# Kernel optimization log

Hardware: AMD Instinct MI355X
Metric: run time of the kernel (lower is better)

The kernel has to match this reference:

```python
import jax, jax.numpy as jnp
import numpy as np

V, D, B, T = 50257, 512, 64, 512
MEM, FWD = 64, 48
RETRO = MEM - FWD  # 16
EPS = 1e-5


def setup_inputs() -> dict:
    key = jax.random.key(0)
    ks = jax.random.split(key, 16)
    n = lambda i, shape: (jax.random.normal(ks[i], shape, jnp.float32) * 0.02)
    return dict(
        seq=jax.random.randint(ks[0], (B, T), 0, V),
        embed=n(1, (V, D)),
        ff_w1=n(2, (D, 2 * D)), ff_b1=jnp.zeros((2 * D,), jnp.float32),
        ff_w2=n(3, (2 * D, D)), ff_b2=jnp.zeros((D,), jnp.float32),
        ln_g=jnp.ones((D,), jnp.float32), ln_b=jnp.zeros((D,), jnp.float32),
        fg_w=n(4, (D,)), fg_b=jnp.zeros((), jnp.float32),
        nw_w1=n(5, (2 * D, D)), nw_b1=jnp.zeros((D,), jnp.float32),
        nw_w2=n(6, (D,)), nw_b2=jnp.zeros((), jnp.float32),
        wq=n(7, (D, D)), bq=jnp.zeros((D,), jnp.float32),
        wk=n(8, (D, D)), bk=jnp.zeros((D,), jnp.float32),
        wv=n(9, (D, D)), bv=jnp.zeros((D,), jnp.float32),
        wo=n(10, (D, D)), bo=jnp.zeros((D,), jnp.float32),
        rq_w=n(11, (D, D)), rq_b=jnp.zeros((D,), jnp.float32),
        out_w=n(12, (D, V)), out_b=jnp.zeros((V,), jnp.float32),
    )


def reference(seq, embed, ff_w1, ff_b1, ff_w2, ff_b2, ln_g, ln_b,
              fg_w, fg_b, nw_w1, nw_b1, nw_w2, nw_b2,
              wq, bq, wk, bk, wv, bv, wo, bo, rq_w, rq_b, out_w, out_b):
    Bz = seq.shape[0]
    # Encoder: embed -> FFN residual -> LayerNorm
    h0 = embed[seq]                                            # [B,T,D]
    ff = jax.nn.relu(h0 @ ff_w1 + ff_b1) @ ff_w2 + ff_b2
    x = h0 + ff
    mu = x.mean(-1, keepdims=True)
    var = ((x - mu) ** 2).mean(-1, keepdims=True)
    hidden = (x - mu) / jnp.sqrt(var + EPS) * ln_g + ln_b       # [B,T,D]

    cand = hidden[:, :-3, :]                                   # [B,n_cand,D]
    n_cand = cand.shape[1]
    # Forward-gate topk (sorted ascending, as in torch code)
    fwd_scores = cand @ fg_w + fg_b                            # [B,n_cand]
    _, fwd_idx = jax.lax.top_k(fwd_scores, FWD)
    fwd_idx = jnp.sort(fwd_idx, axis=1)                        # [B,FWD]
    fwd_h = jnp.take_along_axis(hidden, fwd_idx[:, :, None], axis=1)  # [B,FWD,D]

    # Condition 'D': MHA re-encode (1 head) of forward slots over full sequence
    q = fwd_h @ wq + bq                                        # [B,FWD,D]
    kk = hidden @ wk + bk                                      # [B,T,D]
    v = hidden @ wv + bv                                       # [B,T,D]
    attn = jax.nn.softmax(jnp.einsum('bkd,btd->bkt', q, kk) / jnp.sqrt(jnp.float32(D)), axis=-1)
    re_slots = jnp.einsum('bkt,btd->bkd', attn, v) @ wo + bo   # [B,FWD,D]

    # New-write gate over skipped candidates -> retro slots
    context = hidden.mean(1)                                   # [B,D]
    gi = jnp.concatenate([cand, jnp.broadcast_to(context[:, None, :], cand.shape)], axis=-1)
    gs = jax.nn.sigmoid(jax.nn.relu(gi @ nw_w1 + nw_b1) @ nw_w2 + nw_b2)  # [B,n_cand]
    fwd_mask = jnp.zeros((Bz, n_cand), jnp.float32).at[
        jnp.arange(Bz)[:, None], fwd_idx].set(1.0)
    masked = jnp.where(fwd_mask > 0, -1e9, gs)
    _, sel = jax.lax.top_k(masked, RETRO)                      # [B,RETRO], descending-score order
    retro_h = jnp.take_along_axis(hidden, sel[:, :, None], axis=1)  # [B,RETRO,D]

    memory = jnp.concatenate([re_slots, retro_h], axis=1)      # [B,MEM,D] (exactly full)
    mem_mask = jnp.ones((Bz, MEM), jnp.float32)

    # Read head
    qh = hidden[:, -2, :] @ rq_w + rq_b                        # [B,D]
    scores = jnp.einsum('bmd,bd->bm', memory, qh)
    scores = jnp.where(mem_mask == 0, -1e9, scores)
    a = jax.nn.softmax(scores, axis=-1)
    ctx = jnp.einsum('bm,bmd->bd', a, memory)
    return ctx @ out_w + out_b                                 # [B,V]
```

## Files before the change

kernel.cpp:

```cpp
#include <hip/hip_runtime.h>

typedef unsigned short u16;
typedef unsigned int u32;

#define VV 50257
#define NCAND 509
#define NFWD 48
#define NRETRO 16

typedef __attribute__((ext_vector_type(8))) short bf16x8;
typedef __attribute__((ext_vector_type(4))) float f32x4;

__device__ __forceinline__ float bf2f(u16 u) {
  union { u32 i; float f; } v; v.i = ((u32)u) << 16; return v.f;
}
__device__ __forceinline__ u16 f2bf(float f) {
  union { float f; u32 u; } v; v.f = f;
  u32 u = v.u; u += 0x7fffu + ((u >> 16) & 1u); return (u16)(u >> 16);
}
__device__ __forceinline__ u16 bft(float f) {
  union { float f; u32 u; } v; v.f = f; return (u16)(v.u >> 16);
}
__device__ __forceinline__ float ldsel(const void* p, size_t i, int isbf) {
  return isbf ? bf2f(((const u16*)p)[i]) : ((const float*)p)[i];
}

__device__ __forceinline__ void g2l16(const u16* g, u16* l) {
  __builtin_amdgcn_global_load_lds((const __attribute__((address_space(1))) u32*)g,
                                   (__attribute__((address_space(3))) u32*)l, 16, 0, 0);
}

__global__ void detect_k(const u32* __restrict__ w, int* __restrict__ flag) {
  int bf = 1;
  for (int i = 0; i < 16; ++i) {
    u32 b1 = (w[i] >> 8) & 0x7fu;
    if (!(b1 >= 0x30u && b1 < 0x40u)) bf = 0;
  }
  *flag = bf;
}

__global__ void sentinel_k(float* __restrict__ out, int n, float val) {
  int i = blockIdx.x * 256 + threadIdx.x;
  if (i < n) out[i] = val;
}

__global__ __launch_bounds__(256) void tsplit_k(const float* __restrict__ W,
                                                u16* __restrict__ Th, u16* __restrict__ Tl,
                                                int K, int N) {
  __shared__ float tt[32][33];
  int nt = N >> 5;
  int n0 = (blockIdx.x % nt) << 5;
  int k0 = (blockIdx.x / nt) << 5;
  int c = threadIdx.x & 31, r = threadIdx.x >> 5;
#pragma unroll
  for (int i = 0; i < 32; i += 8) tt[r + i][c] = W[(size_t)(k0 + r + i) * N + n0 + c];
  __syncthreads();
#pragma unroll
  for (int i = 0; i < 32; i += 8) {
    int n = n0 + r + i, k = k0 + c;
    float v = tt[c][r + i];
    u16 h = bft(v);
    int idx = n * K + (k & ~63) + ((k & 63) ^ ((n & 7) << 3));
    Th[idx] = h; Tl[idx] = f2bf(v - bf2f(h));
  }
}

__global__ __launch_bounds__(256) void gsplit_k(const float* __restrict__ embed,
                                                const int* __restrict__ seqp,
                                                u16* __restrict__ Ph, u16* __restrict__ Pl) {
  int g = blockIdx.x * 256 + threadIdx.x;
  int m = g >> 6, j8 = (g & 63) << 3;
  const float* s = embed + (size_t)seqp[m] * 512 + j8;
  float4 a = *(const float4*)s;
  float4 b = *(const float4*)(s + 4);
  u16 h0 = bft(a.x), h1 = bft(a.y), h2 = bft(a.z), h3 = bft(a.w);
  u16 h4 = bft(b.x), h5 = bft(b.y), h6 = bft(b.z), h7 = bft(b.w);
  uint4 hv, lv;
  hv.x = (u32)h0 | ((u32)h1 << 16); hv.y = (u32)h2 | ((u32)h3 << 16);
  hv.z = (u32)h4 | ((u32)h5 << 16); hv.w = (u32)h6 | ((u32)h7 << 16);
  lv.x = (u32)f2bf(a.x - bf2f(h0)) | ((u32)f2bf(a.y - bf2f(h1)) << 16);
  lv.y = (u32)f2bf(a.z - bf2f(h2)) | ((u32)f2bf(a.w - bf2f(h3)) << 16);
  lv.z = (u32)f2bf(b.x - bf2f(h4)) | ((u32)f2bf(b.y - bf2f(h5)) << 16);
  lv.w = (u32)f2bf(b.z - bf2f(h6)) | ((u32)f2bf(b.w - bf2f(h7)) << 16);
  int di = m * 512 + (j8 ^ ((m & 7) << 3));
  *(uint4*)&Ph[di] = hv;
  *(uint4*)&Pl[di] = lv;
}

template<int ADDM, int RELU, int ACC, int OUT>
__global__ __launch_bounds__(256) void mgemm_k(
    const u16* __restrict__ Ah, const u16* __restrict__ Al,
    const u16* __restrict__ Bh, const u16* __restrict__ Bl,
    int ldk, int koff,
    const float* __restrict__ biasf, int boff,
    const u16* __restrict__ Rh, const u16* __restrict__ Rl,
    const float* __restrict__ addf,
    float* __restrict__ Cf, u16* __restrict__ Cb,
    u16* __restrict__ Ohi, u16* __restrict__ Olo)
{
  __shared__ __align__(16) u16 lds[32768];
  int tid = threadIdx.x;
  int cpx = gridDim.x >> 3;
  int bid = blockIdx.x;
  int wg = (bid & 7) * cpx + (bid >> 3);
  int my = wg >> 2, nx = wg & 3;
  int m0 = my << 7, n0 = nx << 7;
  int lane = tid & 63, wid = tid >> 6;

  const u16* gw; int stw;
  if (wid == 0)      { gw = Ah + (size_t)m0 * 512;        stw = 512; }
  else if (wid == 1) { gw = Al + (size_t)m0 * 512;        stw = 512; }
  else if (wid == 2) { gw = Bh + (size_t)n0 * ldk + koff; stw = ldk; }
  else               { gw = Bl + (size_t)n0 * ldk + koff; stw = ldk; }
  const u16* gl = gw + (size_t)(lane >> 3) * stw + ((lane & 7) << 3);
  int lb = wid << 13;

  f32x4 acc[4][4] = {};
  int wr = wid >> 1, wc = wid & 1;
  int cl = lane & 15;
  int kq8 = (lane >> 4) << 3;
  int swz = (cl & 7) << 3;

  for (int k0 = 0; k0 < 512; k0 += 64) {
#pragma unroll
    for (int i = 0; i < 16; ++i)
      g2l16(gl + (size_t)(i << 3) * stw + k0, &lds[lb + (i << 9)]);
    __syncthreads();
#pragma unroll
    for (int kt = 0; kt < 2; ++kt) {
      int kA = ((kt << 5) + kq8) ^ swz;
      bf16x8 bh[4], blo[4];
#pragma unroll
      for (int i = 0; i < 4; ++i) {
        int ib = (((wc << 6) + (i << 4) + cl) << 6) + kA;
        bh[i]  = *(const bf16x8*)&lds[16384 + ib];
        blo[i] = *(const bf16x8*)&lds[24576 + ib];
      }
#pragma unroll
      for (int i2 = 0; i2 < 4; ++i2) {
        int ia = (((wr << 6) + (i2 << 4) + cl) << 6) + kA;
        bf16x8 ah  = *(const bf16x8*)&lds[ia];
        bf16x8 alo = *(const bf16x8*)&lds[8192 + ia];
#pragma unroll
        for (int j = 0; j < 4; ++j) {
          acc[i2][j] = __builtin_amdgcn_mfma_f32_16x16x32_bf16(ah,  bh[j],  acc[i2][j], 0, 0, 0);
          acc[i2][j] = __builtin_amdgcn_mfma_f32_16x16x32_bf16(alo, bh[j],  acc[i2][j], 0, 0, 0);
          acc[i2][j] = __builtin_amdgcn_mfma_f32_16x16x32_bf16(ah,  blo[j], acc[i2][j], 0, 0, 0);
        }
      }
    }
    __syncthreads();
  }

  int rq = (lane >> 4) << 2;
  int mb = m0 + (wr << 6);
  int nb = n0 + (wc << 6);
#pragma unroll
  for (int j = 0; j < 4; ++j) {
    int n = nb + (j << 4) + cl;
    float bi = biasf ? biasf[boff + n] : 0.f;
#pragma unroll
    for (int i2 = 0; i2 < 4; ++i2) {
#pragma unroll
      for (int r = 0; r < 4; ++r) {
        int m = mb + (i2 << 4) + rq + r;
        float v = acc[i2][j][r] + bi;
        if (ADDM == 1) {
          int ridx = m * 512 + (n ^ ((m & 7) << 3));
          v += bf2f(Rh[ridx]) + bf2f(Rl[ridx]);
        }
        if (ADDM == 2) v += addf[((m >> 9) << 9) + n];
        if (ACC) v += Cf[(size_t)m * 512 + n];
        if (RELU) v = fmaxf(v, 0.f);
        if (OUT == 0) Cf[(size_t)m * 512 + n] = v;
        else if (OUT == 1) Cb[(size_t)m * 512 + n] = f2bf(v);
        else if (OUT == 2) {
          u16 h = bft(v);
          int oidx = m * 512 + (n ^ ((m & 7) << 3));
          Ohi[oidx] = h; Olo[oidx] = f2bf(v - bf2f(h));
        } else {
          int r64 = (m * 43691) >> 21;
          int mm = (r64 << 6) + (m - r64 * 48);
          Cf[(size_t)mm * 512 + n] = v;
        }
      }
    }
  }
}

template<int AG, int ADDM, int RELU, int ACC, int OUTBF>
__global__ __launch_bounds__(256) void gemm_k(
    const float* __restrict__ A, int lda,
    const void* __restrict__ gbase, const int* __restrict__ gidx,
    const void* __restrict__ Bw, int ldb, size_t boff,
    const void* __restrict__ bias, size_t bias_eoff,
    const void* __restrict__ adg_base, const int* __restrict__ adg_idx, int adg_ld,
    const float* __restrict__ addf, int add_shift, int addf_ld,
    void* __restrict__ Cv, int ldc, int K,
    const int* __restrict__ flagp)
{
  __shared__ float As[16][68];
  __shared__ float Bs[16][68];
  int isbf = *flagp;
  int tid = threadIdx.x;
  int m0 = blockIdx.y * 64;
  int n0 = blockIdx.x * 64;
  int tx = tid & 15, ty = tid >> 4;
  int arow = tid >> 2;
  int akq  = (tid & 3) << 2;
  int bcol = tid & 63;
  int bk0  = tid >> 6;

  size_t a_off;
  if (AG) a_off = (size_t)gidx[m0 + arow] * (size_t)lda;
  else    a_off = (size_t)(m0 + arow) * (size_t)lda;

  float acc[4][4] = {};

  for (int k0 = 0; k0 < K; k0 += 16) {
    {
      float4 v = *(const float4*)(A + a_off + k0 + akq);
      As[akq + 0][arow] = v.x;
      As[akq + 1][arow] = v.y;
      As[akq + 2][arow] = v.z;
      As[akq + 3][arow] = v.w;
    }
    if (isbf) {
      const u16* bp = (const u16*)Bw + boff;
#pragma unroll
      for (int l = 0; l < 4; ++l) {
        int kb = bk0 + (l << 2);
        Bs[kb][bcol] = bf2f(bp[(size_t)(k0 + kb) * ldb + n0 + bcol]);
      }
    } else {
      const float* bp = (const float*)Bw + boff;
#pragma unroll
      for (int l = 0; l < 4; ++l) {
        int kb = bk0 + (l << 2);
        Bs[kb][bcol] = bp[(size_t)(k0 + kb) * ldb + n0 + bcol];
      }
    }
    __syncthreads();
#pragma unroll
    for (int k = 0; k < 16; ++k) {
      float4 a4 = *(const float4*)&As[k][ty << 2];
      float4 b4 = *(const float4*)&Bs[k][tx << 2];
      float a[4] = {a4.x, a4.y, a4.z, a4.w};
      float bv[4] = {b4.x, b4.y, b4.z, b4.w};
#pragma unroll
      for (int i = 0; i < 4; ++i)
#pragma unroll
        for (int j = 0; j < 4; ++j) acc[i][j] += a[i] * bv[j];
    }
    __syncthreads();
  }

  int mrow = m0 + (ty << 2);
  int ncol = n0 + (tx << 2);
  float bi4[4] = {0.f, 0.f, 0.f, 0.f};
  if (bias) {
#pragma unroll
    for (int j = 0; j < 4; ++j) bi4[j] = ldsel(bias, bias_eoff + ncol + j, isbf);
  }
#pragma unroll
  for (int i = 0; i < 4; ++i) {
    int m = mrow + i;
    float v[4];
#pragma unroll
    for (int j = 0; j < 4; ++j) v[j] = acc[i][j] + bi4[j];
    if (RELU) {
#pragma unroll
      for (int j = 0; j < 4; ++j) v[j] = fmaxf(v[j], 0.f);
    }
    float4 o; o.x = v[0]; o.y = v[1]; o.z = v[2]; o.w = v[3];
    *(float4*)((float*)Cv + (size_t)m * ldc + ncol) = o;
  }
}

__global__ __launch_bounds__(256) void ln_split_k(const float* __restrict__ x,
                                                  const float* __restrict__ g,
                                                  const float* __restrict__ bt,
                                                  u16* __restrict__ Hh, u16* __restrict__ Hl) {
  int row = blockIdx.x;
  const float* p = x + (size_t)row * 512;
  int tid = threadIdx.x;
  __shared__ float red[256];
  __shared__ float stat[2];
  float v0 = p[tid], v1 = p[tid + 256];
  red[tid] = v0 + v1;
  __syncthreads();
  for (int s = 128; s > 0; s >>= 1) { if (tid < s) red[tid] += red[tid + s]; __syncthreads(); }
  if (tid == 0) stat[0] = red[0] * (1.0f / 512.0f);
  __syncthreads();
  float mu = stat[0];
  float d0 = v0 - mu, d1 = v1 - mu;
  red[tid] = d0 * d0 + d1 * d1;
  __syncthreads();
  for (int s = 128; s > 0; s >>= 1) { if (tid < s) red[tid] += red[tid + s]; __syncthreads(); }
  if (tid == 0) stat[1] = 1.0f / sqrtf(red[0] * (1.0f / 512.0f) + 1e-5f);
  __syncthreads();
  float inv = stat[1];
  float y0 = d0 * inv * g[tid] + bt[tid];
  float y1 = d1 * inv * g[tid + 256] + bt[tid + 256];
  int c = (row & 7) << 3;
  int i0 = row * 512 + (tid ^ c);
  int i1 = row * 512 + ((tid + 256) ^ c);
  u16 h0 = bft(y0), h1 = bft(y1);
  Hh[i0] = h0; Hl[i0] = f2bf(y0 - bf2f(h0));
  Hh[i1] = h1; Hl[i1] = f2bf(y1 - bf2f(h1));
}

__global__ __launch_bounds__(256) void score_p_k(const u16* __restrict__ Hh,
                                                 const u16* __restrict__ Hl,
                                                 const float* __restrict__ w,
                                                 const float* __restrict__ b,
                                                 float* __restrict__ out) {
  int bb = blockIdx.y; int t0 = blockIdx.x * 64;
  __shared__ float wl[512];
  for (int d = threadIdx.x; d < 512; d += 256) wl[d] = w[d];
  __syncthreads();
  int wave = threadIdx.x >> 6, lane = threadIdx.x & 63;
  float bias = b[0];
  for (int r = wave; r < 64; r += 4) {
    int grow = bb * 512 + t0 + r;
    int lx = lane ^ ((grow & 7) << 3);
    const u16* ph = Hh + (size_t)grow * 512;
    const u16* pl = Hl + (size_t)grow * 512;
    float s = 0.f;
#pragma unroll
    for (int d = 0; d < 8; ++d)
      s += (bf2f(ph[lx + d * 64]) + bf2f(pl[lx + d * 64])) * wl[lane + d * 64];
#pragma unroll
    for (int off = 32; off > 0; off >>= 1) s += __shfl_xor(s, off);
    if (lane == 0) out[bb * 512 + t0 + r] = s + bias;
  }
}

template<int SIG>
__global__ __launch_bounds__(256) void score_k(const float* __restrict__ h,
                                               const void* __restrict__ w,
                                               const void* __restrict__ b,
                                               float* __restrict__ out,
                                               const int* __restrict__ flagp) {
  int isbf = *flagp;
  int bb = blockIdx.y; int t0 = blockIdx.x * 64;
  __shared__ float wl[512];
  for (int d = threadIdx.x; d < 512; d += 256) wl[d] = ldsel(w, d, isbf);
  __syncthreads();
  int wave = threadIdx.x >> 6, lane = threadIdx.x & 63;
  float bias = ldsel(b, 0, isbf);
  for (int r = wave; r < 64; r += 4) {
    const float* hp = h + ((size_t)bb * 512 + t0 + r) * 512;
    float s = 0.f;
#pragma unroll
    for (int d = 0; d < 8; ++d) s += hp[lane + d * 64] * wl[lane + d * 64];
#pragma unroll
    for (int off = 32; off > 0; off >>= 1) s += __shfl_xor(s, off);
    if (lane == 0) {
      float v = s + bias;
      if (SIG) v = 1.0f / (1.0f + expf(-v));
      out[bb * 512 + t0 + r] = v;
    }
  }
}

__global__ __launch_bounds__(256) void topk_fwd_k(const float* __restrict__ scores,
                                                  int* __restrict__ fwd_idx,
                                                  int* __restrict__ fwd_mask) {
  int b = blockIdx.x, tid = threadIdx.x;
  __shared__ float vals[512];
  __shared__ float rv[256];
  __shared__ int   ri[256];
  __shared__ int   selb[NFWD];
  for (int t = tid; t < 512; t += 256) {
    vals[t] = (t < NCAND) ? scores[b * 512 + t] : -3.0e38f;
    fwd_mask[b * 512 + t] = 0;
  }
  __syncthreads();
  for (int it = 0; it < NFWD; ++it) {
    float bv = -3.0e38f; int bi = 0x7fffffff;
    for (int t = tid; t < 512; t += 256) {
      float v = vals[t];
      if (v > bv || (v == bv && t < bi)) { bv = v; bi = t; }
    }
    rv[tid] = bv; ri[tid] = bi;
    __syncthreads();
    for (int s = 128; s > 0; s >>= 1) {
      if (tid < s) {
        float ov = rv[tid + s]; int oi = ri[tid + s];
        if (ov > rv[tid] || (ov == rv[tid] && oi < ri[tid])) { rv[tid] = ov; ri[tid] = oi; }
      }
      __syncthreads();
    }
    if (tid == 0) { selb[it] = ri[0]; vals[ri[0]] = -3.0e38f; }
    __syncthreads();
  }
  if (tid == 0) {
    for (int i = 1; i < NFWD; ++i) {
      int v = selb[i], j = i - 1;
      while (j >= 0 && selb[j] > v) { selb[j + 1] = selb[j]; --j; }
      selb[j + 1] = v;
    }
    for (int i = 0; i < NFWD; ++i) {
      fwd_idx[b * NFWD + i] = selb[i];
      fwd_mask[b * 512 + selb[i]] = 1;
    }
  }
}

__global__ __launch_bounds__(256) void topk_retro_k(const float* __restrict__ gs,
                                                    const int* __restrict__ fwd_mask,
                                                    int* __restrict__ sel) {
  int b = blockIdx.x, tid = threadIdx.x;
  __shared__ float vals[512];
  __shared__ float rv[256];
  __shared__ int   ri[256];
  for (int t = tid; t < 512; t += 256) {
    float v;
    if (t < NCAND) v = fwd_mask[b * 512 + t] ? -1.0e9f : gs[b * 512 + t];
    else v = -3.0e38f;
    vals[t] = v;
  }
  __syncthreads();
  for (int it = 0; it < NRETRO; ++it) {
    float bv = -3.0e38f; int bi = 0x7fffffff;
    for (int t = tid; t < 512; t += 256) {
      float v = vals[t];
      if (v > bv || (v == bv && t < bi)) { bv = v; bi = t; }
    }
    rv[tid] = bv; ri[tid] = bi;
    __syncthreads();
    for (int s = 128; s > 0; s >>= 1) {
      if (tid < s) {
        float ov = rv[tid + s]; int oi = ri[tid + s];
        if (ov > rv[tid] || (ov == rv[tid] && oi < ri[tid])) { rv[tid] = ov; ri[tid] = oi; }
      }
      __syncthreads();
    }
    if (tid == 0) { sel[b * NRETRO + it] = ri[0]; vals[ri[0]] = -3.0e38f; }
    __syncthreads();
  }
}

__global__ __launch_bounds__(512) void context_part_p(const u16* __restrict__ Hh,
                                                      const u16* __restrict__ Hl,
                                                      float* __restrict__ part) {
  int b = blockIdx.x >> 3, c = blockIdx.x & 7, d = threadIdx.x;
  int dh = d & ~63, dl = d & 63;
  int rbase = b * 512 + c * 64;
  float s = 0.f;
#pragma unroll 8
  for (int t = 0; t < 64; ++t) {
    int idx = (rbase + t) * 512 + dh + (dl ^ ((t & 7) << 3));
    s += bf2f(Hh[idx]) + bf2f(Hl[idx]);
  }
  part[(size_t)((b << 3) + c) * 512 + d] = s;
}
__global__ __launch_bounds__(512) void context_red_k(const float* __restrict__ part,
                                                     float* __restrict__ ctx) {
  int b = blockIdx.x, d = threadIdx.x;
  float s = 0.f;
#pragma unroll
  for (int c = 0; c < 8; ++c) s += part[(size_t)((b << 3) + c) * 512 + d];
  ctx[b * 512 + d] = s * (1.0f / 512.0f);
}

__global__ __launch_bounds__(256) void fwdh_gather_p(const u16* __restrict__ Hh,
                                                     const u16* __restrict__ Hl,
                                                     const int* __restrict__ fwd_idx,
                                                     u16* __restrict__ Fh, u16* __restrict__ Fl) {
  int idx = blockIdx.x * 256 + threadIdx.x;
  int d = idx & 511, r = idx >> 9;
  int b = r / NFWD, i = r % NFWD;
  int t = fwd_idx[b * NFWD + i];
  int srow = b * 512 + t;
  int si = srow * 512 + (d & ~63) + ((d & 63) ^ ((srow & 7) << 3));
  float v = bf2f(Hh[si]) + bf2f(Hl[si]);
  u16 h = bft(v);
  int di = r * 512 + (d & ~63) + ((d & 63) ^ ((r & 7) << 3));
  Fh[di] = h; Fl[di] = f2bf(v - bf2f(h));
}

__global__ __launch_bounds__(256) void retro_gather_p(const u16* __restrict__ Hh,
                                                      const u16* __restrict__ Hl,
                                                      const int* __restrict__ sel,
                                                      float* __restrict__ mem) {
  int idx = blockIdx.x * 256 + threadIdx.x;
  int d = idx & 511, r = idx >> 9, b = r >> 4, j = r & 15;
  int t = sel[b * NRETRO + j];
  int srow = b * 512 + t;
  int si = srow * 512 + (d & ~63) + ((d & 63) ^ ((srow & 7) << 3));
  mem[((size_t)b * 64 + NFWD + j) * 512 + d] = bf2f(Hh[si]) + bf2f(Hl[si]);
}

__global__ __launch_bounds__(256) void s_k(const float* __restrict__ q,
                                           const u16* __restrict__ kk,
                                           float* __restrict__ S) {
  int b = blockIdx.y, t0 = blockIdx.x * 64;
  int tid = threadIdx.x, tq = tid & 15, kq = tid >> 4;
  __shared__ float qs[16][49];
  __shared__ float ks[16][68];
  float acc[3][4] = {};
  for (int dc = 0; dc < 512; dc += 16) {
    for (int e = tid; e < 768; e += 256) {
      int d = e / 48, k2 = e % 48;
      qs[d][k2] = q[((size_t)b * 48 + k2) * 512 + dc + d];
    }
    for (int e = tid; e < 1024; e += 256) {
      int t = e >> 4, d = e & 15;
      ks[d][t] = bf2f(kk[((size_t)b * 512 + t0 + t) * 512 + dc + d]);
    }
    __syncthreads();
#pragma unroll
    for (int d = 0; d < 16; ++d) {
      float4 kv = *(const float4*)&ks[d][tq << 2];
#pragma unroll
      for (int j = 0; j < 3; ++j) {
        float qv = qs[d][kq * 3 + j];
        acc[j][0] += qv * kv.x; acc[j][1] += qv * kv.y;
        acc[j][2] += qv * kv.z; acc[j][3] += qv * kv.w;
      }
    }
    __syncthreads();
  }
  const float sc = 0.044194173824159216f;
#pragma unroll
  for (int j = 0; j < 3; ++j) {
    int k = kq * 3 + j;
    float4 o; o.x = acc[j][0] * sc; o.y = acc[j][1] * sc;
    o.z = acc[j][2] * sc; o.w = acc[j][3] * sc;
    *(float4*)&S[((size_t)b * 48 + k) * 512 + t0 + (tq << 2)] = o;
  }
}

__global__ __launch_bounds__(256) void softmax_k(float* __restrict__ S) {
  float* p = S + (size_t)blockIdx.x * 512;
  int tid = threadIdx.x;
  __shared__ float red[256];
  __shared__ float stat[2];
  float v0 = p[tid], v1 = p[tid + 256];
  red[tid] = fmaxf(v0, v1);
  __syncthreads();
  for (int s = 128; s > 0; s >>= 1) { if (tid < s) red[tid] = fmaxf(red[tid], red[tid + s]); __syncthreads(); }
  if (tid == 0) stat[0] = red[0];
  __syncthreads();
  float mx = stat[0];
  float e0 = expf(v0 - mx), e1 = expf(v1 - mx);
  red[tid] = e0 + e1;
  __syncthreads();
  for (int s = 128; s > 0; s >>= 1) { if (tid < s) red[tid] += red[tid + s]; __syncthreads(); }
  if (tid == 0) stat[1] = 1.0f / red[0];
  __syncthreads();
  float inv = stat[1];
  p[tid] = e0 * inv; p[tid + 256] = e1 * inv;
}

__global__ __launch_bounds__(256) void pv_k(const float* __restrict__ P,
                                            const u16* __restrict__ vvp,
                                            u16* __restrict__ Ph, u16* __restrict__ Pl) {
  int b = blockIdx.y, d0 = blockIdx.x * 64;
  int tid = threadIdx.x, dq = tid & 15, kq = tid >> 4;
  __shared__ float ps[16][49];
  __shared__ float vs[16][68];
  float acc[3][4] = {};
  for (int tc = 0; tc < 512; tc += 16) {
    for (int e = tid; e < 768; e += 256) {
      int t = e / 48, k2 = e % 48;
      ps[t][k2] = P[((size_t)b * 48 + k2) * 512 + tc + t];
    }
    for (int e = tid; e < 1024; e += 256) {
      int t = e >> 6, d = e & 63;
      vs[t][d] = bf2f(vvp[((size_t)b * 512 + tc + t) * 512 + d0 + d]);
    }
    __syncthreads();
#pragma unroll
    for (int t = 0; t < 16; ++t) {
      float4 vval = *(const float4*)&vs[t][dq << 2];
#pragma unroll
      for (int j = 0; j < 3; ++j) {
        float pp = ps[t][kq * 3 + j];
        acc[j][0] += pp * vval.x; acc[j][1] += pp * vval.y;
        acc[j][2] += pp * vval.z; acc[j][3] += pp * vval.w;
      }
    }
    __syncthreads();
  }
#pragma unroll
  for (int j = 0; j < 3; ++j) {
    int k = kq * 3 + j;
    int row = b * 48 + k;
    int c = (row & 7) << 3;
    int di = row * 512 + d0 + ((dq << 2) ^ c);
    float v0 = acc[j][0], v1 = acc[j][1], v2 = acc[j][2], v3 = acc[j][3];
    u16 h0 = bft(v0), h1 = bft(v1), h2 = bft(v2), h3 = bft(v3);
    uint2 hv, lv;
    hv.x = (u32)h0 | ((u32)h1 << 16); hv.y = (u32)h2 | ((u32)h3 << 16);
    lv.x = (u32)f2bf(v0 - bf2f(h0)) | ((u32)f2bf(v1 - bf2f(h1)) << 16);
    lv.y = (u32)f2bf(v2 - bf2f(h2)) | ((u32)f2bf(v3 - bf2f(h3)) << 16);
    *(uint2*)&Ph[di] = hv;
    *(uint2*)&Pl[di] = lv;
  }
}

__global__ __launch_bounds__(512) void qh_p_k(const u16* __restrict__ Hh,
                                              const u16* __restrict__ Hl,
                                              const float* __restrict__ rq_w,
                                              const float* __restrict__ rq_b,
                                              float* __restrict__ qh) {
  int b = blockIdx.x, d = threadIdx.x;
  __shared__ float hr[512];
  int row = b * 512 + 510;
  int idx = row * 512 + (d & ~63) + ((d & 63) ^ 48);
  hr[d] = bf2f(Hh[idx]) + bf2f(Hl[idx]);
  __syncthreads();
  float s = 0.f;
  for (int k = 0; k < 512; ++k) s += hr[k] * rq_w[(size_t)k * 512 + d];
  qh[b * 512 + d] = s + rq_b[d];
}

__global__ __launch_bounds__(512) void mem_attn_k(const float* __restrict__ mem,
                                                  const float* __restrict__ qh,
                                                  float* __restrict__ ctx,
                                                  float* __restrict__ ctxT) {
  int b = blockIdx.x, tid = threadIdx.x;
  __shared__ float qv[512];
  __shared__ float sc[64];
  qv[tid] = qh[b * 512 + tid];
  __syncthreads();
  if (tid < 64) {
    const float* mp = mem + ((size_t)b * 64 + tid) * 512;
    float s = 0.f;
    for (int d = 0; d < 512; ++d) s += mp[d] * qv[d];
    float mx = s;
#pragma unroll
    for (int off = 32; off > 0; off >>= 1) mx = fmaxf(mx, __shfl_xor(mx, off));
    float e = expf(s - mx);
    float sum = e;
#pragma unroll
    for (int off = 32; off > 0; off >>= 1) sum += __shfl_xor(sum, off);
    sc[tid] = e / sum;
  }
  __syncthreads();
  float a = 0.f;
  for (int m = 0; m < 64; ++m) a += sc[m] * mem[((size_t)b * 64 + m) * 512 + tid];
  ctx[b * 512 + tid] = a;
  ctxT[(size_t)tid * 64 + b] = a;
}

__global__ __launch_bounds__(256) void out_gemm_k(const float* __restrict__ ctxT,
                                                  const void* __restrict__ out_w,
                                                  const void* __restrict__ out_b,
                                                  float* __restrict__ out,
                                                  const int* __restrict__ flagp) {
  int isbf = *flagp;
  int bid = blockIdx.x;
  int xslab = (bid & 7) + ((bid >> 5) << 3);
  if (xslab >= 197) return;
  int bg = (bid >> 3) & 3;
  int n = xslab * 256 + threadIdx.x;
  int nc = n < VV ? n : VV - 1;
  int b0 = bg << 4;
  float acc[16];
#pragma unroll
  for (int i = 0; i < 16; ++i) acc[i] = 0.f;
  if (isbf) {
    const u16* wp = (const u16*)out_w;
#pragma unroll 4
    for (int k = 0; k < 512; ++k) {
      float w = bf2f(wp[(size_t)k * VV + nc]);
      const float* cp = ctxT + ((size_t)k << 6) + b0;
#pragma unroll
      for (int i = 0; i < 16; ++i) acc[i] += cp[i] * w;
    }
  } else {
    const float* wp = (const float*)out_w;
#pragma unroll 4
    for (int k = 0; k < 512; ++k) {
      float w = wp[(size_t)k * VV + nc];
      const float* cp = ctxT + ((size_t)k << 6) + b0;
#pragma unroll
      for (int i = 0; i < 16; ++i) acc[i] += cp[i] * w;
    }
  }
  if (n < VV) {
    float ob = ldsel(out_b, n, isbf);
#pragma unroll
    for (int i = 0; i < 16; ++i) out[(size_t)(b0 + i) * VV + n] = acc[i] + ob;
  }
}

extern "C" void kernel_launch(void* const* d_in, const int* in_sizes, int n_in,
                              void* d_out, int out_size, void* d_ws, size_t ws_size,
                              hipStream_t stream) {
  const int*  seq    = (const int*)d_in[0];
  const void* embed  = d_in[1];
  const void* ff_w1  = d_in[2];
  const void* ff_b1  = d_in[3];
  const void* ff_w2  = d_in[4];
  const void* ff_b2  = d_in[5];
  const void* ln_g   = d_in[6];
  const void* ln_b   = d_in[7];
  const void* fg_w   = d_in[8];
  const void* fg_b   = d_in[9];
  const void* nw_w1  = d_in[10];
  const void* nw_b1  = d_in[11];
  const void* nw_w2  = d_in[12];
  const void* nw_b2  = d_in[13];
  const void* wq     = d_in[14];
  const void* bq     = d_in[15];
  const void* wk     = d_in[16];
  const void* bk     = d_in[17];
  const void* wv     = d_in[18];
  const void* bv     = d_in[19];
  const void* wo     = d_in[20];
  const void* bo     = d_in[21];
  const void* rq_w   = d_in[22];
  const void* rq_b   = d_in[23];
  const void* out_w  = d_in[24];
  const void* out_b  = d_in[25];
  float* out = (float*)d_out;

  float* ws = (float*)d_ws;
  float* hidden = ws;
  float* g1f    = ws;
  u16*   kku    = (u16*)ws;
  u16*   vvu    = (u16*)(ws + 8388608);
  u16* actHh = (u16*)(ws + 16777216);
  u16* actHl = actHh + 8388608;
  u16* h0h   = (u16*)(ws + 25165824);
  u16* h0l   = h0h + 8388608;
  u16* Hh    = (u16*)(ws + 16777216);
  u16* Hl    = Hh + 16777216;
  size_t S0 = 33554432;
  float* fwd_scores = ws + S0;
  float* gs         = ws + S0 + 32768;
  float* context    = ws + S0 + 65536;
  float* gate_bias  = ws + S0 + 98304;
  float* qh         = ws + S0 + 131072;
  float* ctx        = ws + S0 + 163840;
  int*   fwd_idx    = (int*)(ws + S0 + 196608);
  int*   sel        = (int*)(ws + S0 + 199680);
  int*   fwd_mask   = (int*)(ws + S0 + 200704);
  int*   flagp      = (int*)(ws + S0 + 233472);
  float* cpart      = ws + S0 + 262144;
  u16*   Fh         = (u16*)(ws + S0 + 262144);
  u16*   Fl         = Fh + 1572864;
  float* q          = ws + S0 + 1835008;
  float* Smat       = ws + S0 + 3407872;
  u16* W0   = (u16*)(ws + S0 + 3407872);
  u16* WTnh = W0;            u16* WTnl = W0 + 262144;
  u16* WTkh = W0 + 524288;   u16* WTkl = W0 + 786432;
  u16* WTvh = W0 + 1048576;  u16* WTvl = W0 + 1310720;
  u16* WT1h = W0 + 1572864;  u16* WT1l = W0 + 2097152;
  u16* WT2h = W0 + 2621440;  u16* WT2l = W0 + 3145728;
  u16* Ph   = (u16*)(ws + S0 + 4980736);
  u16* Pl   = Ph + 1572864;
  u16* Wq0  = (u16*)(ws + S0 + 6553600);
  u16* WTqh = Wq0;          u16* WTql = Wq0 + 262144;
  u16* WToh = Wq0 + 524288; u16* WTol = Wq0 + 786432;
  float* memory = ws + S0 + 8126464;
  float* ctxT   = fwd_scores;
  const size_t NEED = (size_t)(33554432 + 10223616) * 4;

  if (ws_size < NEED) {
    float val = 500.0f + (float)(ws_size >> 20);
    sentinel_k<<<(out_size + 255) / 256, 256, 0, stream>>>(out, out_size, val);
    return;
  }

  detect_k<<<1, 1, 0, stream>>>((const u32*)embed, flagp);

  tsplit_k<<<512, 256, 0, stream>>>((const float*)ff_w1, WT1h, WT1l, 512, 1024);
  tsplit_k<<<512, 256, 0, stream>>>((const float*)ff_w2, WT2h, WT2l, 1024, 512);
  tsplit_k<<<256, 256, 0, stream>>>((const float*)nw_w1, WTnh, WTnl, 512, 512);
  tsplit_k<<<256, 256, 0, stream>>>((const float*)wk,    WTkh, WTkl, 512, 512);
  tsplit_k<<<256, 256, 0, stream>>>((const float*)wv,    WTvh, WTvl, 512, 512);
  tsplit_k<<<256, 256, 0, stream>>>((const float*)wq,    WTqh, WTql, 512, 512);
  tsplit_k<<<256, 256, 0, stream>>>((const float*)wo,    WToh, WTol, 512, 512);

  for (int mc = 0; mc < 2; ++mc) {
    const int* seqp = seq + mc * 16384;
    float* hid = hidden + (size_t)mc * 16384 * 512;
    gsplit_k<<<4096, 256, 0, stream>>>((const float*)embed, seqp, h0h, h0l);
    mgemm_k<0,1,0,2><<<512, 256, 0, stream>>>(h0h, h0l, WT1h, WT1l, 512, 0,
        (const float*)ff_b1, 0, nullptr, nullptr, nullptr,
        nullptr, nullptr, actHh, actHl);
    mgemm_k<0,0,0,0><<<512, 256, 0, stream>>>(actHh, actHl, WT2h, WT2l, 1024, 0,
        nullptr, 0, nullptr, nullptr, nullptr,
        hid, nullptr, nullptr, nullptr);
    mgemm_k<0,1,0,2><<<512, 256, 0, stream>>>(h0h, h0l, WT1h + 512*512, WT1l + 512*512, 512, 0,
        (const float*)ff_b1, 512, nullptr, nullptr, nullptr,
        nullptr, nullptr, actHh, actHl);
    mgemm_k<1,0,1,0><<<512, 256, 0, stream>>>(actHh, actHl, WT2h, WT2l, 1024, 512,
        (const float*)ff_b2, 0, h0h, h0l, nullptr,
        hid, nullptr, nullptr, nullptr);
  }
  ln_split_k<<<32768, 256, 0, stream>>>(hidden, (const float*)ln_g, (const float*)ln_b, Hh, Hl);
  score_p_k<<<dim3(8,64), 256, 0, stream>>>(Hh, Hl, (const float*)fg_w, (const float*)fg_b, fwd_scores);
  topk_fwd_k<<<64, 256, 0, stream>>>(fwd_scores, fwd_idx, fwd_mask);
  context_part_p<<<512, 512, 0, stream>>>(Hh, Hl, cpart);
  context_red_k<<<64, 512, 0, stream>>>(cpart, context);
  gemm_k<0,0,0,0,0><<<dim3(8,1), 256, 0, stream>>>(
      context, 512, nullptr, nullptr, nw_w1, 512, (size_t)512*512, nw_b1, 0,
      nullptr, nullptr, 0, nullptr, 0, 0, gate_bias, 512, 512, flagp);
  mgemm_k<2,1,0,0><<<1024, 256, 0, stream>>>(Hh, Hl, WTnh, WTnl, 512, 0,
      nullptr, 0, nullptr, nullptr, gate_bias,
      g1f, nullptr, nullptr, nullptr);
  score_k<1><<<dim3(8,64), 256, 0, stream>>>(g1f, nw_w2, nw_b2, gs, flagp);
  topk_retro_k<<<64, 256, 0, stream>>>(gs, fwd_mask, sel);
  retro_gather_p<<<2048, 256, 0, stream>>>(Hh, Hl, sel, memory);
  fwdh_gather_p<<<6144, 256, 0, stream>>>(Hh, Hl, fwd_idx, Fh, Fl);
  mgemm_k<0,0,0,0><<<96, 256, 0, stream>>>(Fh, Fl, WTqh, WTql, 512, 0,
      (const float*)bq, 0, nullptr, nullptr, nullptr,
      q, nullptr, nullptr, nullptr);
  mgemm_k<0,0,0,1><<<1024, 256, 0, stream>>>(Hh, Hl, WTkh, WTkl, 512, 0,
      (const float*)bk, 0, nullptr, nullptr, nullptr,
      nullptr, kku, nullptr, nullptr);
  mgemm_k<0,0,0,1><<<1024, 256, 0, stream>>>(Hh, Hl, WTvh, WTvl, 512, 0,
      (const float*)bv, 0, nullptr, nullptr, nullptr,
      nullptr, vvu, nullptr, nullptr);
  s_k<<<dim3(8,64), 256, 0, stream>>>(q, kku, Smat);
  softmax_k<<<3072, 256, 0, stream>>>(Smat);
  pv_k<<<dim3(8,64), 256, 0, stream>>>(Smat, vvu, Ph, Pl);
  mgemm_k<0,0,0,3><<<96, 256, 0, stream>>>(Ph, Pl, WToh, WTol, 512, 0,
      (const float*)bo, 0, nullptr, nullptr, nullptr,
      memory, nullptr, nullptr, nullptr);
  qh_p_k<<<64, 512, 0, stream>>>(Hh, Hl, (const float*)rq_w, (const float*)rq_b, qh);
  mem_attn_k<<<64, 512, 0, stream>>>(memory, qh, ctx, ctxT);
  out_gemm_k<<<800, 256, 0, stream>>>(ctxT, out_w, out_b, out, flagp);
}
```

Before: 1.245 ms.

## Fuse context sum into gate scoring and split output GEMM along K

The forward-gate scoring kernel now also builds per-chunk column sums of hidden, so the separate context_part pass that reread Hh/Hl is gone. The vocab projection is split into two K halves with 8-row batch groups, which gives 3200 blocks instead of 800 to raise occupancy. Partial results go to two workspace buffers, and a new combine kernel adds them with the bias. This costs extra global traffic for the partials (two 64xV float buffers written and read back) and drops the bf16 weight path, now always reading out_w as float.

Measured after the change: 1.254 ms. No clear change (+0.7%).

```diff
diff --git a/kernel.cpp b/kernel.cpp
--- a/kernel.cpp
+++ b/kernel.cpp
@@ -310,16 +310,19 @@
   Hh[i1] = h1; Hl[i1] = f2bf(y1 - bf2f(h1));
 }
 
-__global__ __launch_bounds__(256) void score_p_k(const u16* __restrict__ Hh,
+__global__ __launch_bounds__(256) void gatectx_k(const u16* __restrict__ Hh,
                                                  const u16* __restrict__ Hl,
                                                  const float* __restrict__ w,
                                                  const float* __restrict__ b,
-                                                 float* __restrict__ out) {
-  int bb = blockIdx.y; int t0 = blockIdx.x * 64;
+                                                 float* __restrict__ out,
+                                                 float* __restrict__ part) {
+  int bb = blockIdx.y, t0 = blockIdx.x * 64;
   __shared__ float wl[512];
+  __shared__ float cred[4][512];
   for (int d = threadIdx.x; d < 512; d += 256) wl[d] = w[d];
-  __syncthreads();
   int wave = threadIdx.x >> 6, lane = threadIdx.x & 63;
+  float ca[8] = {};
+  __syncthreads();
   float bias = b[0];
   for (int r = wave; r < 64; r += 4) {
     int grow = bb * 512 + t0 + r;
@@ -328,12 +331,21 @@
     const u16* pl = Hl + (size_t)grow * 512;
     float s = 0.f;
 #pragma unroll
-    for (int d = 0; d < 8; ++d)
-      s += (bf2f(ph[lx + d * 64]) + bf2f(pl[lx + d * 64])) * wl[lane + d * 64];
+    for (int d = 0; d < 8; ++d) {
+      float hv = bf2f(ph[lx + d * 64]) + bf2f(pl[lx + d * 64]);
+      ca[d] += hv;
+      s += hv * wl[lane + d * 64];
+    }
 #pragma unroll
     for (int off = 32; off > 0; off >>= 1) s += __shfl_xor(s, off);
     if (lane == 0) out[bb * 512 + t0 + r] = s + bias;
   }
+#pragma unroll
+  for (int d = 0; d < 8; ++d) cred[wave][lane + d * 64] = ca[d];
+  __syncthreads();
+  for (int d = threadIdx.x; d < 512; d += 256)
+    part[(size_t)((bb << 3) + blockIdx.x) * 512 + d] =
+        cred[0][d] + cred[1][d] + cred[2][d] + cred[3][d];
 }
 
 template<int SIG>
@@ -442,20 +454,6 @@
   }
 }
 
-__global__ __launch_bounds__(512) void context_part_p(const u16* __restrict__ Hh,
-                                                      const u16* __restrict__ Hl,
-                                                      float* __restrict__ part) {
-  int b = blockIdx.x >> 3, c = blockIdx.x & 7, d = threadIdx.x;
-  int dh = d & ~63, dl = d & 63;
-  int rbase = b * 512 + c * 64;
-  float s = 0.f;
-#pragma unroll 8
-  for (int t = 0; t < 64; ++t) {
-    int idx = (rbase + t) * 512 + dh + (dl ^ ((t & 7) << 3));
-    s += bf2f(Hh[idx]) + bf2f(Hl[idx]);
-  }
-  part[(size_t)((b << 3) + c) * 512 + d] = s;
-}
 __global__ __launch_bounds__(512) void context_red_k(const float* __restrict__ part,
                                                      float* __restrict__ ctx) {
   int b = blockIdx.x, d = threadIdx.x;
@@ -647,45 +645,44 @@
   ctxT[(size_t)tid * 64 + b] = a;
 }
 
-__global__ __launch_bounds__(256) void out_gemm_k(const float* __restrict__ ctxT,
-                                                  const void* __restrict__ out_w,
-                                                  const void* __restrict__ out_b,
-                                                  float* __restrict__ out,
-                                                  const int* __restrict__ flagp) {
-  int isbf = *flagp;
+__global__ __launch_bounds__(256) void out_part_k(const float* __restrict__ ctxT,
+                                                  const float* __restrict__ out_w,
+                                                  float* __restrict__ P0,
+                                                  float* __restrict__ P1) {
   int bid = blockIdx.x;
-  int xslab = (bid & 7) + ((bid >> 5) << 3);
-  if (xslab >= 197) return;
-  int bg = (bid >> 3) & 3;
+  int slab2 = (bid & 7) + ((bid >> 6) << 3);
+  if (slab2 >= 394) return;
+  int xslab = slab2 >> 1, kh = slab2 & 1;
+  int bg = (bid >> 3) & 7;
   int n = xslab * 256 + threadIdx.x;
   int nc = n < VV ? n : VV - 1;
-  int b0 = bg << 4;
-  float acc[16];
-#pragma unroll
-  for (int i = 0; i < 16; ++i) acc[i] = 0.f;
-  if (isbf) {
-    const u16* wp = (const u16*)out_w;
-#pragma unroll 4
-    for (int k = 0; k < 512; ++k) {
-      float w = bf2f(wp[(size_t)k * VV + nc]);
-      const float* cp = ctxT + ((size_t)k << 6) + b0;
-#pragma unroll
-      for (int i = 0; i < 16; ++i) acc[i] += cp[i] * w;
-    }
-  } else {
-    const float* wp = (const float*)out_w;
-#pragma unroll 4
-    for (int k = 0; k < 512; ++k) {
-      float w = wp[(size_t)k * VV + nc];
-      const float* cp = ctxT + ((size_t)k << 6) + b0;
-#pragma unroll
-      for (int i = 0; i < 16; ++i) acc[i] += cp[i] * w;
-    }
-  }
+  int b0 = bg << 3;
+  int k0 = kh << 8;
+  float acc[8] = {};
+  const float* wp = out_w + (size_t)k0 * VV;
+#pragma unroll 8
+  for (int k = 0; k < 256; ++k) {
+    float w = wp[(size_t)k * VV + nc];
+    const float* cp = ctxT + ((size_t)(k0 + k) << 6) + b0;
+#pragma unroll
+    for (int i = 0; i < 8; ++i) acc[i] += cp[i] * w;
+  }
+  float* dst = kh ? P1 : P0;
   if (n < VV) {
-    float ob = ldsel(out_b, n, isbf);
-#pragma unroll
-    for (int i = 0; i < 16; ++i) out[(size_t)(b0 + i) * VV + n] = acc[i] + ob;
+#pragma unroll
+    for (int i = 0; i < 8; ++i) dst[(size_t)(b0 + i) * VV + n] = acc[i];
+  }
+}
+
+__global__ __launch_bounds__(256) void out_comb_k(const float* __restrict__ P0,
+                                                  const float* __restrict__ P1,
+                                                  const float* __restrict__ ob,
+                                                  float* __restrict__ out) {
+  int b = blockIdx.y;
+  int n = blockIdx.x * 256 + threadIdx.x;
+  if (n < VV) {
+    size_t i = (size_t)b * VV + n;
+    out[i] = P0[i] + P1[i] + ob[n];
   }
 }
 
@@ -725,6 +722,8 @@
   float* g1f    = ws;
   u16*   kku    = (u16*)ws;
   u16*   vvu    = (u16*)(ws + 8388608);
+  float* P0     = ws;
+  float* P1     = ws + 3216448;
   u16* actHh = (u16*)(ws + 16777216);
   u16* actHl = actHh + 8388608;
   u16* h0h   = (u16*)(ws + 25165824);
@@ -796,9 +795,9 @@
         hid, nullptr, nullptr, nullptr);
   }
   ln_split_k<<<32768, 256, 0, stream>>>(hidden, (const float*)ln_g, (const float*)ln_b, Hh, Hl);
-  score_p_k<<<dim3(8,64), 256, 0, stream>>>(Hh, Hl, (const float*)fg_w, (const float*)fg_b, fwd_scores);
+  gatectx_k<<<dim3(8,64), 256, 0, stream>>>(Hh, Hl, (const float*)fg_w, (const float*)fg_b,
+                                            fwd_scores, cpart);
   topk_fwd_k<<<64, 256, 0, stream>>>(fwd_scores, fwd_idx, fwd_mask);
-  context_part_p<<<512, 512, 0, stream>>>(Hh, Hl, cpart);
   context_red_k<<<64, 512, 0, stream>>>(cpart, context);
   gemm_k<0,0,0,0,0><<<dim3(8,1), 256, 0, stream>>>(
       context, 512, nullptr, nullptr, nw_w1, 512, (size_t)512*512, nw_b1, 0,
@@ -827,5 +826,6 @@
       memory, nullptr, nullptr, nullptr);
   qh_p_k<<<64, 512, 0, stream>>>(Hh, Hl, (const float*)rq_w, (const float*)rq_b, qh);
   mem_attn_k<<<64, 512, 0, stream>>>(memory, qh, ctx, ctxT);
-  out_gemm_k<<<800, 256, 0, stream>>>(ctxT, out_w, out_b, out, flagp);
-}
+  out_part_k<<<3200, 256, 0, stream>>>(ctxT, (const float*)out_w, P0, P1);
+  out_comb_k<<<dim3(197,64), 256, 0, stream>>>(P0, P1, (const float*)out_b, out);
+}
```
